# Optimization experiments

Measured on AMD Instinct MI355X. Metric: run time of the kernel, lower is better.

## Reference

```python
import jax, jax.numpy as jnp
import numpy as np

D_MODEL = 64; D_INNER = 64; D_STATE = 8; DT_RANK = 4; D_CONV = 4
B, C, H, W = 16, 1024, 32, 32


def _silu(x):
    return x * jax.nn.sigmoid(x)


def _layernorm(x, g, b, eps=1e-5):
    m = x.mean(-1, keepdims=True)
    v = ((x - m) ** 2).mean(-1, keepdims=True)
    return (x - m) * jax.lax.rsqrt(v + eps) * g + b


def _rmsnorm(x, w, eps=1e-5):
    return x * jax.lax.rsqrt((x * x).mean(-1, keepdims=True) + eps) * w


def _causal_conv1d(x, w, b):
    # x: [B, D, L]; depthwise causal conv, kernel w: [D, K]
    D = x.shape[1]; K = w.shape[1]
    xp = jnp.pad(x, ((0, 0), (0, 0), (K - 1, 0)))
    y = jax.lax.conv_general_dilated(xp, w[:, None, :], (1,), 'VALID',
                                     dimension_numbers=('NCH', 'OIH', 'NCH'),
                                     feature_group_count=D)
    return y + b[None, :, None]


def _selective_scan(x, z, A_log, Dvec, xproj_w, dt_w, dt_b):
    # x, z: [B, D, L]
    A = -jnp.exp(A_log)                                    # [D, N]
    xdb = jnp.einsum('bdl,kd->blk', x, xproj_w)            # [B, L, R+2N]
    dt_lr = xdb[..., :DT_RANK]
    Bc = xdb[..., DT_RANK:DT_RANK + D_STATE]               # [B, L, N]
    Cc = xdb[..., DT_RANK + D_STATE:]                      # [B, L, N]
    dt = jax.nn.softplus(jnp.einsum('blr,dr->bld', dt_lr, dt_w) + dt_b)  # [B, L, D]
    dA = jnp.exp(dt[..., None] * A[None, None])            # [B, L, D, N]
    dBx = dt[..., None] * Bc[:, :, None, :] * x.transpose(0, 2, 1)[..., None]  # [B, L, D, N]

    def step(h, inp):
        dA_t, dBx_t, C_t = inp
        h = dA_t * h + dBx_t                               # [B, D, N]
        return h, jnp.einsum('bdn,bn->bd', h, C_t)

    h0 = jnp.zeros((x.shape[0], x.shape[1], D_STATE), x.dtype)
    _, ys = jax.lax.scan(step, h0, (dA.transpose(1, 0, 2, 3),
                                    dBx.transpose(1, 0, 2, 3),
                                    Cc.transpose(1, 0, 2)))
    y = ys.transpose(1, 2, 0) + Dvec[None, :, None] * x    # [B, D, L]
    return y * _silu(z)


def _mamba_branch(u, in_w, conv_w, conv_b, xproj_w, dt_w, dt_b, A_log, Dvec):
    # u: [B, L, d_model]
    xz = jnp.einsum('bld,ed->bel', u, in_w)                # [B, 2*D_INNER, L]
    x, z = jnp.split(xz, 2, axis=1)
    x = _silu(_causal_conv1d(x, conv_w, conv_b))
    return _selective_scan(x, z, A_log, Dvec, xproj_w, dt_w, dt_b)


def setup_inputs():
    key = jax.random.key(0)
    ks = jax.random.split(key, 20)
    rn = lambda i, shape, s=1.0: jax.random.normal(ks[i], shape, dtype=jnp.float32) * s
    s4d = jnp.log(jnp.tile(jnp.arange(1, D_STATE + 1, dtype=jnp.float32)[None, :], (D_INNER, 1)))
    return {
        'img1': rn(0, (B, C, H, W)),
        'img2': rn(1, (B, C, H, W)),
        'pre_w': rn(2, (D_MODEL, 1), 0.3),
        'pre_b': rn(3, (D_MODEL,), 0.1),
        'ln_g': jnp.ones((D_MODEL,), jnp.float32),
        'ln_b': jnp.zeros((D_MODEL,), jnp.float32),
        'in_w': rn(4, (2 * D_INNER, D_MODEL), 0.1),
        'in_b_w': rn(5, (2 * D_INNER, D_MODEL), 0.1),
        'conv_w': rn(6, (D_INNER, D_CONV), 0.3),
        'conv_bias': rn(7, (D_INNER,), 0.1),
        'convb_w': rn(8, (D_INNER, D_CONV), 0.3),
        'convb_bias': rn(9, (D_INNER,), 0.1),
        'xproj_w': rn(10, (DT_RANK + 2 * D_STATE, D_INNER), 0.1),
        'xprojb_w': rn(11, (DT_RANK + 2 * D_STATE, D_INNER), 0.1),
        'dt_w': rn(12, (D_INNER, DT_RANK), 0.1),
        'dt_bias': rn(13, (D_INNER,), 0.1),
        'dtb_w': rn(14, (D_INNER, DT_RANK), 0.1),
        'dtb_bias': rn(15, (D_INNER,), 0.1),
        'A_log': s4d,
        'A_b_log': s4d,
        'Dp': jnp.ones((D_INNER,), jnp.float32),
        'Dp_b': jnp.ones((D_INNER,), jnp.float32),
        'norm_w': jnp.ones((D_INNER,), jnp.float32),
        'out_w': rn(16, (D_MODEL, D_INNER), 0.1),
        'post_w': rn(17, (1, D_MODEL), 0.3),
        'post_b': jnp.zeros((1,), jnp.float32),
    }


def reference(img1, img2, pre_w, pre_b, ln_g, ln_b, in_w, in_b_w, conv_w, conv_bias,
              convb_w, convb_bias, xproj_w, xprojb_w, dt_w, dt_bias, dtb_w, dtb_bias,
              A_log, A_b_log, Dp, Dp_b, norm_w, out_w, post_w, post_b):
    # AdaptiveMaxPool2d((1,1)) + squeeze(-1) -> [B, C, 1]
    p1 = jnp.max(img1, axis=(2, 3))[..., None]
    p2 = jnp.max(img2, axis=(2, 3))[..., None]
    # pre_linear: Linear(1, 64) then LayerNorm(64)  -> [B, C(=L), 64]
    x1 = _layernorm(p1 * pre_w[:, 0] + pre_b, ln_g, ln_b)
    x2 = _layernorm(p2 * pre_w[:, 0] + pre_b, ln_g, ln_b)
    # bimamba v3 (cross): forward scan on x1, reversed scan on extra_emb=x2
    out_f = _mamba_branch(x1, in_w, conv_w, conv_bias, xproj_w, dt_w, dt_bias, A_log, Dp)
    out_b = _mamba_branch(x2[:, ::-1, :], in_b_w, convb_w, convb_bias, xprojb_w,
                          dtb_w, dtb_bias, A_b_log, Dp_b)[:, :, ::-1]
    y = (out_f + out_b).transpose(0, 2, 1)                 # [B, L, D_INNER]
    y = _rmsnorm(y, norm_w)                                # use_norm=True
    y = jnp.einsum('bld,ed->ble', y, out_w)                # out_proj (no bias)
    att = jnp.einsum('bld,od->blo', y, post_w) + post_b    # post_linear -> [B, C, 1]
    return jax.nn.sigmoid(att[..., None])                  # [B, C, 1, 1]
```

## Files before the change

### kernel.cpp

```cpp
#include <hip/hip_runtime.h>
#include <math.h>

typedef float f32x4 __attribute__((ext_vector_type(4)));

#define NCH 32
#define CLN 32

#define OFF_P   0
#define OFF_Q   524288
#define OFF_DTT 1048576
#define OFF_SXT 3145728
#define OFF_BCT 5242880
#define OFF_AN  5767168
#define OFF_HIN 5832704
#define OFF_WZ  6356992
#define OFF_VEW 6357376
#define OFF_AL2 6357440

#define LOG2E 1.4426950408889634f
#define LN2   0.6931471805599453f

__device__ __forceinline__ float fexp2(float x){ return __builtin_amdgcn_exp2f(x); }
__device__ __forceinline__ float flog2(float x){ return __builtin_amdgcn_logf(x); }
__device__ __forceinline__ float frcp (float x){ return __builtin_amdgcn_rcpf(x); }
__device__ __forceinline__ float fsigmoid(float x){ return frcp(1.f + fexp2(-x*LOG2E)); }
__device__ __forceinline__ float fsilu(float x){ return x * fsigmoid(x); }
__device__ __forceinline__ float fsoftplus(float x){
  return fmaxf(x, 0.f) + LN2 * flog2(1.f + fexp2(-fabsf(x)*LOG2E));
}

__device__ __forceinline__ float wave_rsum(float v){
  #pragma unroll
  for (int o = 1; o < 64; o <<= 1) v += __shfl_xor(v, o, 64);
  return v;
}
__device__ __forceinline__ float wave_rmax(float v){
  #pragma unroll
  for (int o = 1; o < 64; o <<= 1) v = fmaxf(v, __shfl_xor(v, o, 64));
  return v;
}

struct Smem {
  float a1[36], a2[36], a3[36];
  float xpt[20*65];
  float dtlr[32*4];
  float sxt[64*37];
  float dtt[32*64];
  float bct[32*16];
  float gw[64], gb[64], lnbs[64];
  float W[384];
  float cst[4];
};

__device__ __forceinline__ void consts_ln(float* gw, float* gb, float* lnbs, float* cst, int t,
    const float* pre_w, const float* pre_b, const float* ln_g, const float* ln_b){
  if (t < 64){
    float w = pre_w[t], b = pre_b[t];
    float mw = wave_rsum(w) * (1.f/64.f);
    float mb = wave_rsum(b) * (1.f/64.f);
    float wc = w - mw, bc = b - mb;
    float Av = wave_rsum(wc*wc) * (1.f/64.f);
    float Bq = wave_rsum(wc*bc) * (1.f/64.f);
    float Cq = wave_rsum(bc*bc) * (1.f/64.f);
    gw[t] = wc * ln_g[t];
    gb[t] = bc * ln_g[t];
    lnbs[t] = ln_b[t];
    if (t == 0){ cst[0] = Av; cst[1] = Bq; cst[2] = Cq; }
  }
}

__device__ __forceinline__ void proj_body(
    Smem& S, int t,
    const float* __restrict__ cw, const float* __restrict__ cb,
    const float* __restrict__ xpw, const float* __restrict__ dw,
    const float* __restrict__ dbv){
  for (int i = t; i < 20*64; i += 512){
    int k = i >> 6, d = i & 63;
    S.xpt[k*65 + d] = xpw[i];
  }
  __syncthreads();
  {
    int d = t & 63, lq = t >> 6;
    float cw0=cw[d*4], cw1=cw[d*4+1], cw2=cw[d*4+2], cw3=cw[d*4+3];
    float cbd = cb[d];
    float W1d = S.W[d], W2d = S.W[128+d], W3d = S.W[256+d];
    #pragma unroll
    for (int j = 0; j < 4; ++j){
      int ll = lq*4 + j;
      float A1 = cw0*S.a1[ll] + cw1*S.a1[ll+1] + cw2*S.a1[ll+2] + cw3*S.a1[ll+3];
      float A2 = cw0*S.a2[ll] + cw1*S.a2[ll+1] + cw2*S.a2[ll+2] + cw3*S.a2[ll+3];
      float A3 = cw0*S.a3[ll] + cw1*S.a3[ll+1] + cw2*S.a3[ll+2] + cw3*S.a3[ll+3];
      float xc = W1d*A1 + W2d*A2 + W3d*A3 + cbd;
      S.sxt[d*37 + ll] = fsilu(xc);
    }
  }
  __syncthreads();
  {
    int ll = t >> 4, k = t & 15;
    float acc = 0.f;
    #pragma unroll 8
    for (int d = 0; d < 64; ++d) acc += S.xpt[(4+k)*65 + d] * S.sxt[d*37 + ll];
    S.bct[ll*16 + k] = acc;
  }
  if (t < 128){
    int ll = t >> 2, r = t & 3;
    float acc = 0.f;
    #pragma unroll 8
    for (int d = 0; d < 64; ++d) acc += S.xpt[r*65 + d] * S.sxt[d*37 + ll];
    S.dtlr[ll*4 + r] = acc;
  }
  __syncthreads();
  {
    int d = t & 63, lq = t >> 6;
    float w0=dw[d*4], w1=dw[d*4+1], w2=dw[d*4+2], w3=dw[d*4+3];
    float bd = dbv[d];
    #pragma unroll
    for (int j = 0; j < 4; ++j){
      int ll = lq*4 + j;
      float raw = bd + w0*S.dtlr[ll*4] + w1*S.dtlr[ll*4+1]
                     + w2*S.dtlr[ll*4+2] + w3*S.dtlr[ll*4+3];
      S.dtt[ll*64 + d] = fsoftplus(raw);
    }
  }
  __syncthreads();
}

__global__ void __launch_bounds__(512) k_projA(
    const float* __restrict__ img1, const float* __restrict__ img2,
    const float* pre_w, const float* pre_b, const float* ln_g, const float* ln_b,
    const float* in_w, const float* in_b_w, const float* A_log, const float* A_b_log,
    const float* conv_w, const float* conv_b, const float* convb_w, const float* convb_b,
    const float* xproj_w, const float* xprojb_w,
    const float* dt_w, const float* dt_b, const float* dtb_w, const float* dtb_b,
    const float* norm_w, const float* out_w, const float* post_w,
    float* __restrict__ ws){
  __shared__ __align__(16) Smem S;
  int bi = blockIdx.x;
  int c = bi & 31, bq = bi >> 5, br = bq >> 4, b = bq & 15;
  int t = threadIdx.x;
  int wv = t >> 6, lane = t & 63;
  const float* img = br ? img2 : img1;
  #pragma unroll
  for (int k = 0; k < 5; ++k){
    int i = wv + k*8;
    if (i < 35){
      bool valid = (c > 0) || (i >= 3);
      if (valid){
        int l = br ? (1026 - c*32 - i) : (c*32 - 3 + i);
        const f32x4* rp = (const f32x4*)(img + ((size_t)(b*1024 + l))*1024) + lane;
        f32x4 q0 = __builtin_nontemporal_load(rp +   0);
        f32x4 q1 = __builtin_nontemporal_load(rp +  64);
        f32x4 q2 = __builtin_nontemporal_load(rp + 128);
        f32x4 q3 = __builtin_nontemporal_load(rp + 192);
        float m = fmaxf(fmaxf(fmaxf(q0.x,q0.y), fmaxf(q0.z,q0.w)),
                        fmaxf(fmaxf(q1.x,q1.y), fmaxf(q1.z,q1.w)));
        m = fmaxf(m, fmaxf(fmaxf(fmaxf(q2.x,q2.y), fmaxf(q2.z,q2.w)),
                           fmaxf(fmaxf(q3.x,q3.y), fmaxf(q3.z,q3.w))));
        m = wave_rmax(m);
        if (lane == 0) S.a1[i] = m;
      } else if (lane == 0) S.a1[i] = 0.f;
    }
  }
  consts_ln(S.gw, S.gb, S.lnbs, S.cst, t, pre_w, pre_b, ln_g, ln_b);
  __syncthreads();
  if (t < 128){
    const float* iw = br ? in_b_w : in_w;
    float s1 = 0.f, s2 = 0.f, s3 = 0.f;
    #pragma unroll 8
    for (int d = 0; d < 64; ++d){
      float w = iw[t*64 + d];
      s1 += w * S.gw[d]; s2 += w * S.gb[d]; s3 += w * S.lnbs[d];
    }
    S.W[      t] = s1;
    S.W[128 + t] = s2;
    S.W[256 + t] = s3;
  }
  float A2r = -fexp2((br ? A_b_log : A_log)[t] * LOG2E) * LOG2E;
  __syncthreads();
  if (t < 36){
    bool ok = (t < 35) && ((c > 0) || (t >= 3));
    float m = ok ? S.a1[t] : 0.f;
    float Av = S.cst[0], Bq = S.cst[1], Cq = S.cst[2];
    float inv = rsqrtf(m*m*Av + 2.f*m*Bq + Cq + 1e-5f);
    S.a1[t] = ok ? m*inv : 0.f;
    S.a2[t] = ok ? inv   : 0.f;
    S.a3[t] = ok ? 1.f   : 0.f;
  }
  proj_body(S, t,
            br ? convb_w : conv_w,  br ? convb_b : conv_b,
            br ? xprojb_w : xproj_w, br ? dtb_w : dt_w, br ? dtb_b : dt_b);
  {
    int dd = t >> 3, tt0 = (t & 7)*4;
    f32x4 sv; sv.x = S.sxt[dd*37+tt0];   sv.y = S.sxt[dd*37+tt0+1];
              sv.z = S.sxt[dd*37+tt0+2]; sv.w = S.sxt[dd*37+tt0+3];
    *(f32x4*)(ws + OFF_SXT + (size_t)bi*2048 + dd*32 + tt0) = sv;
    f32x4 dv; dv.x = S.dtt[t*4];   dv.y = S.dtt[t*4+1];
              dv.z = S.dtt[t*4+2]; dv.w = S.dtt[t*4+3];
    *(f32x4*)(ws + OFF_DTT + (size_t)bi*2048 + t*4) = dv;
    if (t < 128){
      f32x4 bv; bv.x = S.bct[t*4];   bv.y = S.bct[t*4+1];
                bv.z = S.bct[t*4+2]; bv.w = S.bct[t*4+3];
      *(f32x4*)(ws + OFF_BCT + (size_t)bi*512 + t*4) = bv;
    }
    if (t < 32){
      ws[OFF_AN + (size_t)bi*64 + t]      = S.a1[t+3];
      ws[OFF_AN + (size_t)bi*64 + 32 + t] = S.a2[t+3];
    }
  }
  if (bi == 0 || bi == 512){
    ws[OFF_AL2 + br*512 + t] = A2r;
    if (t < 64){
      ws[OFF_WZ + br*192 +       t] = S.W[64 + t];
      ws[OFF_WZ + br*192 +  64 + t] = S.W[128 + 64 + t];
      ws[OFF_WZ + br*192 + 128 + t] = S.W[256 + 64 + t];
    }
    if (bi == 0 && t < 64){
      float s = 0.f;
      #pragma unroll 8
      for (int e = 0; e < 64; ++e) s += post_w[e] * out_w[e*64 + t];
      ws[OFF_VEW + t] = s * norm_w[t];
    }
  }
  int d = wv*8 + (lane >> 3), n = lane & 7;
  float P = 1.f, Q = 0.f;
  #pragma unroll 4
  for (int tt = 0; tt < CLN; ++tt){
    float dtv = S.dtt[tt*64 + d];
    float xv  = S.sxt[d*37 + tt];
    float bv  = S.bct[tt*16 + n];
    float da  = fexp2(dtv * A2r);
    Q = fmaf(da, Q, dtv * bv * xv);
    P *= da;
  }
  ws[OFF_P + (size_t)bi*512 + t] = P;
  ws[OFF_Q + (size_t)bi*512 + t] = Q;
}

__global__ void __launch_bounds__(64) k_scanB(float* __restrict__ ws){
  int gid = blockIdx.x*64 + threadIdx.x;
  int bq = gid >> 9, dn = gid & 511;
  size_t base = (size_t)bq*NCH*512 + dn;
  float P[NCH], Q[NCH];
  #pragma unroll
  for (int c = 0; c < NCH; ++c){
    P[c] = ws[OFF_P + base + (size_t)c*512];
    Q[c] = ws[OFF_Q + base + (size_t)c*512];
  }
  float h = 0.f;
  #pragma unroll
  for (int c = 0; c < NCH; ++c){
    ws[OFF_HIN + base + (size_t)c*512] = h;
    h = fmaf(P[c], h, Q[c]);
  }
}

__global__ void __launch_bounds__(1024) k_scanY(
    const float* Dp, const float* Dp_b, const float* post_b,
    const float* __restrict__ ws, float* __restrict__ out){
  __shared__ __align__(16) struct {
    float dtt[2][2048];
    float sxt[2][2368];
    float bct[2][512];
    float an[2][64];
    float ylds[2][CLN*65];
  } C;
  int bi = blockIdx.x;
  int oc = bi & 31, b = bi >> 5;
  int t = threadIdx.x;
  int team = t >> 9, u = t & 511;
  int lane = t & 63;
  int wv_all = t >> 6;
  int d = ((u >> 6) << 3) + ((u & 63) >> 3), n = u & 7;
  int ti = team ? ((b+16)*32 + (31 - oc)) : (b*32 + oc);
  f32x4 dv = *(const f32x4*)(ws + OFF_DTT + (size_t)ti*2048 + u*4);
  f32x4 sv = *(const f32x4*)(ws + OFF_SXT + (size_t)ti*2048 + u*4);
  float h   = ws[OFF_HIN + (size_t)ti*512 + u];
  float A2r = ws[OFF_AL2 + team*512 + u];
  float W1z = ws[OFF_WZ + team*192 +       d];
  float W2z = ws[OFF_WZ + team*192 +  64 + d];
  float W3z = ws[OFF_WZ + team*192 + 128 + d];
  float Dpd = (team ? Dp_b : Dp)[d];
  float ve  = ws[OFF_VEW + lane];
  float pb  = post_b[0];
  f32x4 bv4, av4;
  if (u < 128) bv4 = *(const f32x4*)(ws + OFF_BCT + (size_t)ti*512 + u*4);
  if (u < 16)  av4 = *(const f32x4*)(ws + OFF_AN  + (size_t)ti*64  + u*4);
  {
    *(f32x4*)&C.dtt[team][u*4] = dv;
    int dd = u >> 3, tt0 = (u & 7)*4;
    C.sxt[team][dd*37+tt0+0] = sv.x; C.sxt[team][dd*37+tt0+1] = sv.y;
    C.sxt[team][dd*37+tt0+2] = sv.z; C.sxt[team][dd*37+tt0+3] = sv.w;
    if (u < 128) *(f32x4*)&C.bct[team][u*4] = bv4;
    if (u < 16)  *(f32x4*)&C.an[team][u*4]  = av4;
  }
  __syncthreads();
  {
    const float* dtt = C.dtt[team];
    const float* sxt = C.sxt[team];
    const float* bct = C.bct[team];
    const float* an  = C.an[team];
    float* yl = C.ylds[team];
    #pragma unroll 4
    for (int tt = 0; tt < CLN; ++tt){
      float dtv = dtt[tt*64 + d];
      float xv  = sxt[d*37 + tt];
      float bv  = bct[tt*16 + n];
      float cv  = bct[tt*16 + 8 + n];
      float da  = fexp2(dtv * A2r);
      h = fmaf(da, h, dtv * bv * xv);
      float pv = h * cv;
      pv += __shfl_xor(pv, 1, 64);
      pv += __shfl_xor(pv, 2, 64);
      pv += __shfl_xor(pv, 4, 64);
      if (n == 0){
        float y = pv + Dpd * xv;
        float zv = an[tt]*W1z + an[32+tt]*W2z + W3z;
        float g = fsilu(zv);
        int row = team ? (31 - tt) : tt;
        yl[row*65 + d] = y * g;
      }
    }
  }
  __syncthreads();
  #pragma unroll
  for (int j = 0; j < 2; ++j){
    int row = wv_all*2 + j;
    float v = C.ylds[0][row*65 + lane] + C.ylds[1][row*65 + lane];
    float ss = v*v, dp = v*ve;
    #pragma unroll
    for (int o = 1; o < 64; o <<= 1){
      ss += __shfl_xor(ss, o, 64);
      dp += __shfl_xor(dp, o, 64);
    }
    if (lane == 0){
      float rstd = rsqrtf(ss*(1.f/64.f) + 1e-5f);
      out[b*1024 + oc*32 + row] = fsigmoid(dp*rstd + pb);
    }
  }
}

extern "C" void kernel_launch(void* const* d_in, const int* in_sizes, int n_in,
                              void* d_out, int out_size, void* d_ws, size_t ws_size,
                              hipStream_t stream){
  const float* img1      = (const float*)d_in[0];
  const float* img2      = (const float*)d_in[1];
  const float* pre_w     = (const float*)d_in[2];
  const float* pre_b     = (const float*)d_in[3];
  const float* ln_g      = (const float*)d_in[4];
  const float* ln_b      = (const float*)d_in[5];
  const float* in_w      = (const float*)d_in[6];
  const float* in_b_w    = (const float*)d_in[7];
  const float* conv_w    = (const float*)d_in[8];
  const float* conv_bias = (const float*)d_in[9];
  const float* convb_w   = (const float*)d_in[10];
  const float* convb_bias= (const float*)d_in[11];
  const float* xproj_w   = (const float*)d_in[12];
  const float* xprojb_w  = (const float*)d_in[13];
  const float* dt_w      = (const float*)d_in[14];
  const float* dt_bias   = (const float*)d_in[15];
  const float* dtb_w     = (const float*)d_in[16];
  const float* dtb_bias  = (const float*)d_in[17];
  const float* A_log     = (const float*)d_in[18];
  const float* A_b_log   = (const float*)d_in[19];
  const float* Dp        = (const float*)d_in[20];
  const float* Dp_b      = (const float*)d_in[21];
  const float* norm_w    = (const float*)d_in[22];
  const float* out_w     = (const float*)d_in[23];
  const float* post_w    = (const float*)d_in[24];
  const float* post_b    = (const float*)d_in[25];
  float* ws  = (float*)d_ws;
  float* out = (float*)d_out;

  k_projA<<<1024, 512, 0, stream>>>(img1, img2, pre_w, pre_b, ln_g, ln_b,
                                    in_w, in_b_w, A_log, A_b_log,
                                    conv_w, conv_bias, convb_w, convb_bias,
                                    xproj_w, xprojb_w, dt_w, dt_bias, dtb_w, dtb_bias,
                                    norm_w, out_w, post_w, ws);
  k_scanB<<<256, 64, 0, stream>>>(ws);
  k_scanY<<<512, 1024, 0, stream>>>(Dp, Dp_b, post_b, ws, out);
}
```

Measured before the change: 69.95 us.

## Store intermediate dt/x/BC tiles in fp16 and enlarge scanB blocks

The per-chunk dt, conv-x and B/C tiles passed from the projection kernel to the scan kernel are now stored in global workspace as fp16 and widened back to fp32 on load. This halves the workspace traffic between the two kernels. The workspace layout is compacted to match. The chunk-carry kernel also moves from 256 blocks of 64 threads to 64 blocks of 256 threads. The fp16 rounding of dt and x reduces accuracy in the scan, and the chunk-carry P/Q are still computed from the fp32 values, so they no longer match exactly what the scan kernel replays.

```diff
diff --git a/kernel.cpp b/kernel.cpp
--- a/kernel.cpp
+++ b/kernel.cpp
@@ -1,21 +1,23 @@
 #include <hip/hip_runtime.h>
 #include <math.h>
 
-typedef float f32x4 __attribute__((ext_vector_type(4)));
+typedef float    f32x4 __attribute__((ext_vector_type(4)));
+typedef _Float16 f16x4 __attribute__((ext_vector_type(4)));
 
 #define NCH 32
 #define CLN 32
 
-#define OFF_P   0
-#define OFF_Q   524288
-#define OFF_DTT 1048576
-#define OFF_SXT 3145728
-#define OFF_BCT 5242880
-#define OFF_AN  5767168
-#define OFF_HIN 5832704
-#define OFF_WZ  6356992
-#define OFF_VEW 6357376
-#define OFF_AL2 6357440
+#define OFF_P     0
+#define OFF_Q     524288
+#define OFF_HIN   1048576
+#define OFF_AN    1572864
+#define OFF_WZ    1638400
+#define OFF_VEW   1638784
+#define OFF_AL2   1638848
+#define OFF_TILEH 1640448
+#define DTT_H 0
+#define SXT_H 2097152
+#define BCT_H 4194304
 
 #define LOG2E 1.4426950408889634f
 #define LN2   0.6931471805599453f
@@ -190,17 +192,21 @@
             br ? convb_w : conv_w,  br ? convb_b : conv_b,
             br ? xprojb_w : xproj_w, br ? dtb_w : dt_w, br ? dtb_b : dt_b);
   {
+    _Float16* th = (_Float16*)(ws + OFF_TILEH);
     int dd = t >> 3, tt0 = (t & 7)*4;
     f32x4 sv; sv.x = S.sxt[dd*37+tt0];   sv.y = S.sxt[dd*37+tt0+1];
               sv.z = S.sxt[dd*37+tt0+2]; sv.w = S.sxt[dd*37+tt0+3];
-    *(f32x4*)(ws + OFF_SXT + (size_t)bi*2048 + dd*32 + tt0) = sv;
+    *(f16x4*)(th + SXT_H + (size_t)bi*2048 + dd*32 + tt0) =
+        __builtin_convertvector(sv, f16x4);
     f32x4 dv; dv.x = S.dtt[t*4];   dv.y = S.dtt[t*4+1];
               dv.z = S.dtt[t*4+2]; dv.w = S.dtt[t*4+3];
-    *(f32x4*)(ws + OFF_DTT + (size_t)bi*2048 + t*4) = dv;
+    *(f16x4*)(th + DTT_H + (size_t)bi*2048 + t*4) =
+        __builtin_convertvector(dv, f16x4);
     if (t < 128){
       f32x4 bv; bv.x = S.bct[t*4];   bv.y = S.bct[t*4+1];
                 bv.z = S.bct[t*4+2]; bv.w = S.bct[t*4+3];
-      *(f32x4*)(ws + OFF_BCT + (size_t)bi*512 + t*4) = bv;
+      *(f16x4*)(th + BCT_H + (size_t)bi*512 + t*4) =
+          __builtin_convertvector(bv, f16x4);
     }
     if (t < 32){
       ws[OFF_AN + (size_t)bi*64 + t]      = S.a1[t+3];
@@ -236,8 +242,8 @@
   ws[OFF_Q + (size_t)bi*512 + t] = Q;
 }
 
-__global__ void __launch_bounds__(64) k_scanB(float* __restrict__ ws){
-  int gid = blockIdx.x*64 + threadIdx.x;
+__global__ void __launch_bounds__(256) k_scanB(float* __restrict__ ws){
+  int gid = blockIdx.x*256 + threadIdx.x;
   int bq = gid >> 9, dn = gid & 511;
   size_t base = (size_t)bq*NCH*512 + dn;
   float P[NCH], Q[NCH];
@@ -272,8 +278,9 @@
   int wv_all = t >> 6;
   int d = ((u >> 6) << 3) + ((u & 63) >> 3), n = u & 7;
   int ti = team ? ((b+16)*32 + (31 - oc)) : (b*32 + oc);
-  f32x4 dv = *(const f32x4*)(ws + OFF_DTT + (size_t)ti*2048 + u*4);
-  f32x4 sv = *(const f32x4*)(ws + OFF_SXT + (size_t)ti*2048 + u*4);
+  const _Float16* th = (const _Float16*)(ws + OFF_TILEH);
+  f16x4 dvh = *(const f16x4*)(th + DTT_H + (size_t)ti*2048 + u*4);
+  f16x4 svh = *(const f16x4*)(th + SXT_H + (size_t)ti*2048 + u*4);
   float h   = ws[OFF_HIN + (size_t)ti*512 + u];
   float A2r = ws[OFF_AL2 + team*512 + u];
   float W1z = ws[OFF_WZ + team*192 +       d];
@@ -282,15 +289,21 @@
   float Dpd = (team ? Dp_b : Dp)[d];
   float ve  = ws[OFF_VEW + lane];
   float pb  = post_b[0];
-  f32x4 bv4, av4;
-  if (u < 128) bv4 = *(const f32x4*)(ws + OFF_BCT + (size_t)ti*512 + u*4);
-  if (u < 16)  av4 = *(const f32x4*)(ws + OFF_AN  + (size_t)ti*64  + u*4);
-  {
+  f16x4 bvh;
+  f32x4 av4;
+  if (u < 128) bvh = *(const f16x4*)(th + BCT_H + (size_t)ti*512 + u*4);
+  if (u < 16)  av4 = *(const f32x4*)(ws + OFF_AN + (size_t)ti*64 + u*4);
+  {
+    f32x4 dv = __builtin_convertvector(dvh, f32x4);
+    f32x4 sv = __builtin_convertvector(svh, f32x4);
     *(f32x4*)&C.dtt[team][u*4] = dv;
     int dd = u >> 3, tt0 = (u & 7)*4;
     C.sxt[team][dd*37+tt0+0] = sv.x; C.sxt[team][dd*37+tt0+1] = sv.y;
     C.sxt[team][dd*37+tt0+2] = sv.z; C.sxt[team][dd*37+tt0+3] = sv.w;
-    if (u < 128) *(f32x4*)&C.bct[team][u*4] = bv4;
+    if (u < 128){
+      f32x4 bv = __builtin_convertvector(bvh, f32x4);
+      *(f32x4*)&C.bct[team][u*4] = bv;
+    }
     if (u < 16)  *(f32x4*)&C.an[team][u*4]  = av4;
   }
   __syncthreads();
@@ -376,6 +389,6 @@
                                     conv_w, conv_bias, convb_w, convb_bias,
                                     xproj_w, xprojb_w, dt_w, dt_bias, dtb_w, dtb_bias,
                                     norm_w, out_w, post_w, ws);
-  k_scanB<<<256, 64, 0, stream>>>(ws);
+  k_scanB<<<64, 256, 0, stream>>>(ws);
   k_scanY<<<512, 1024, 0, stream>>>(Dp, Dp_b, post_b, ws, out);
 }
```

Result: no change. 68.88 us (-1.5%).
